# Optimization experiments

Hardware: AMD Instinct MI355X
Metric: run time of the kernel (lower is better)

## Reference

```python
import jax, jax.numpy as jnp
import numpy as np
from jax import lax

K = 512   # codebook size
D = 32    # latent dim == encoder out channels
DN = ('NCHW', 'OIHW', 'NCHW')


def _conv(x, w, b, stride):
    y = lax.conv_general_dilated(x, w, (stride, stride), ((1, 1), (1, 1)),
                                 dimension_numbers=DN)
    return y + b[None, :, None, None]


def _deconv(x, w, b):
    # torch ConvTranspose2d(k=4, s=2, p=1); weight layout (in, out, kh, kw).
    # Equivalent: conv with lhs_dilation=2, pad k-1-p = 2, spatially flipped,
    # in/out-swapped kernel.
    rhs = jnp.transpose(jnp.flip(w, (2, 3)), (1, 0, 2, 3))
    y = lax.conv_general_dilated(x, rhs, (1, 1), ((2, 2), (2, 2)),
                                 lhs_dilation=(2, 2), dimension_numbers=DN)
    return y + b[None, :, None, None]


def _forward(imgs, w1, b1, w2, b2, codebook, dw1, db1, dw2, db2):
    # Encoder
    h = jax.nn.relu(_conv(imgs, w1, b1, 2))
    z_e = jax.nn.relu(_conv(h, w2, b2, 2))          # (B, 32, H/4, W/4)
    # Vector quantize
    z = jnp.transpose(z_e, (0, 2, 3, 1))            # (B, h, w, D)
    flat = z.reshape(-1, D)                          # (N, D)
    dist = (jnp.sum(flat * flat, axis=1, keepdims=True)
            + jnp.sum(codebook * codebook, axis=1)
            - 2.0 * flat @ codebook.T)               # (N, K)
    q = jnp.argmin(dist, axis=1)                     # (N,)
    z_q = codebook[q].reshape(z.shape)               # gather == one-hot matmul
    codebook_loss = jnp.mean((lax.stop_gradient(z_q) - z) ** 2)
    commit_loss = jnp.mean((z_q - lax.stop_gradient(z)) ** 2)
    vq_loss = codebook_loss + commit_loss
    z_q_st = z + lax.stop_gradient(z_q - z)          # straight-through
    encoded = jnp.transpose(z_q_st, (0, 3, 1, 2))    # (B, 32, h, w)
    # Decoder
    d = jax.nn.relu(_deconv(encoded, dw1, db1))
    decoded = jax.nn.relu(_deconv(d, dw2, db2))
    return encoded, decoded, vq_loss


def setup_inputs() -> dict:
    key = jax.random.key(0)
    ks = jax.random.split(key, 8)

    def w_init(k, shape):
        fan_in = shape[1] * shape[2] * shape[3]
        bound = 1.0 / np.sqrt(fan_in)
        return jax.random.uniform(k, shape, jnp.float32, -bound, bound)

    imgs = jax.random.normal(ks[0], (32, 3, 256, 256), jnp.float32)
    w1 = w_init(ks[1], (16, 3, 4, 4));  b1 = jnp.zeros((16,), jnp.float32)
    w2 = w_init(ks[2], (32, 16, 4, 4)); b2 = jnp.zeros((32,), jnp.float32)
    # decoder ConvTranspose2d weights, torch layout (in, out, kh, kw)
    dw1 = w_init(ks[3], (32, 16, 4, 4)); db1 = jnp.zeros((16,), jnp.float32)
    dw2 = w_init(ks[4], (16, 3, 4, 4));  db2 = jnp.zeros((3,), jnp.float32)
    codebook = jax.random.uniform(ks[5], (K, D), jnp.float32, -1.0 / K, 1.0 / K)
    return dict(imgs=imgs, w1=w1, b1=b1, w2=w2, b2=b2, codebook=codebook,
                dw1=dw1, db1=db1, dw2=dw2, db2=db2)


def reference(imgs, w1, b1, w2, b2, codebook, dw1, db1, dw2, db2):
    return _forward(imgs, w1, b1, w2, b2, codebook, dw1, db1, dw2, db2)
```

## Files before the change

kernel.cpp:

```cpp
#include <hip/hip_runtime.h>
#include <float.h>

#pragma clang fp contract(off)

__device__ __forceinline__ float pw32(const float* p) {
  float r0 = p[0], r1 = p[1], r2 = p[2], r3 = p[3];
  float r4 = p[4], r5 = p[5], r6 = p[6], r7 = p[7];
  r0 += p[8];  r1 += p[9];  r2 += p[10]; r3 += p[11];
  r4 += p[12]; r5 += p[13]; r6 += p[14]; r7 += p[15];
  r0 += p[16]; r1 += p[17]; r2 += p[18]; r3 += p[19];
  r4 += p[20]; r5 += p[21]; r6 += p[22]; r7 += p[23];
  r0 += p[24]; r1 += p[25]; r2 += p[26]; r3 += p[27];
  r4 += p[28]; r5 += p[29]; r6 += p[30]; r7 += p[31];
  return ((r0 + r1) + (r2 + r3)) + ((r4 + r5) + (r6 + r7));
}

__global__ __launch_bounds__(256) void k_prep(
    const float* __restrict__ w1, const float* __restrict__ w2,
    const float* __restrict__ cb, float* __restrict__ w1t,
    float* __restrict__ w2t, float* __restrict__ bnG) {
  int t = threadIdx.x;
  for (int i = t; i < 8192; i += 256) {
    int tap = i >> 5, co = i & 31;
    w2t[i] = w2[co * 256 + tap];
  }
  for (int i = t; i < 768; i += 256) {
    int tap = i >> 4, co = i & 15;
    w1t[i] = w1[co * 48 + tap];
  }
  for (int k = t; k < 512; k += 256) {
    float p[32];
    #pragma unroll
    for (int d = 0; d < 32; d++) { float c = cb[k * 32 + d]; p[d] = c * c; }
    bnG[k] = pw32(p);
  }
}

__global__ __launch_bounds__(256) void k_conv1(
    const float* __restrict__ img, const float* __restrict__ w1t,
    const float* __restrict__ b1, float* __restrict__ h1, int b0) {
  int idx = blockIdx.x * 256 + threadIdx.x;
  int x  = idx & 127;
  int y  = (idx >> 7) & 127;
  int bl = idx >> 14;
  const float* im = img + (long)(b0 + bl) * 196608;
  float acc[16];
  #pragma unroll
  for (int q = 0; q < 16; q++) acc[q] = 0.f;
  int iy0 = 2 * y - 1, ix0 = 2 * x - 1;
  for (int ci = 0; ci < 3; ci++) {
    const float* imc = im + ci * 65536;
    for (int r = 0; r < 4; r++) {
      int iy = iy0 + r;
      if ((unsigned)iy >= 256u) continue;
      const float* row = imc + iy * 256;
      for (int c = 0; c < 4; c++) {
        int ix = ix0 + c;
        float hv = ((unsigned)ix < 256u) ? row[ix] : 0.f;
        const float* wp = w1t + ((ci * 16 + r * 4 + c) << 4);
        #pragma unroll
        for (int co = 0; co < 16; co++)
          acc[co] = fmaf(hv, wp[co], acc[co]);
      }
    }
  }
  long hbase = (long)bl * 262144 + y * 128 + x;
  #pragma unroll
  for (int co = 0; co < 16; co++)
    h1[hbase + (long)co * 16384] = fmaxf(acc[co] + b1[co], 0.f);
}

__global__ __launch_bounds__(256, 3) void k_conv2z(
    const float* __restrict__ h1, const float* __restrict__ w2t,
    const float* __restrict__ b2, float* __restrict__ enct, int b0) {
  int t = threadIdx.x;
  int half = blockIdx.x & 1;
  int coff = half << 4;
  int ppix = (blockIdx.x >> 1) * 256 + t;
  int x  = ppix & 63;
  int y  = (ppix >> 6) & 63;
  int bl = ppix >> 12;
  int bg = b0 + bl;

  float z[16];
  #pragma unroll
  for (int q = 0; q < 16; q++) z[q] = 0.f;

  int iy0 = 2 * y - 1, ix0 = 2 * x - 1;
  for (int ci = 0; ci < 16; ci++) {
    long hbase = (long)bl * 262144 + (long)ci * 16384;
    for (int r = 0; r < 4; r++) {
      int iy = iy0 + r;
      if ((unsigned)iy >= 128u) continue;
      const float* hrow = h1 + hbase + (long)iy * 128;
      const float* wrow = w2t + ((ci * 16 + r * 4) << 5) + coff;
      for (int c = 0; c < 4; c++) {
        int ix = ix0 + c;
        float hv = ((unsigned)ix < 128u) ? hrow[ix] : 0.f;
        const float* wp = wrow + (c << 5);
        #pragma unroll
        for (int co = 0; co < 16; co++)
          z[co] = fmaf(hv, wp[co], z[co]);
      }
    }
  }
  float4* et4 = (float4*)(enct + ((long)bg * 4096 + y * 64 + x) * 32 + coff);
  #pragma unroll
  for (int d4 = 0; d4 < 4; d4++) {
    float4 v;
    v.x = fmaxf(z[d4 * 4 + 0] + b2[coff + d4 * 4 + 0], 0.f);
    v.y = fmaxf(z[d4 * 4 + 1] + b2[coff + d4 * 4 + 1], 0.f);
    v.z = fmaxf(z[d4 * 4 + 2] + b2[coff + d4 * 4 + 2], 0.f);
    v.w = fmaxf(z[d4 * 4 + 3] + b2[coff + d4 * 4 + 3], 0.f);
    et4[d4] = v;
  }
}

template <int W>
__device__ __forceinline__ double vq_epi(const float* cw, const float (&z)[32],
                                         float* __restrict__ enc, long ebase,
                                         float4* et4) {
  int d = W * 4;
  float f0 = cw[d + 0] - z[d + 0], e0 = z[d + 0] + f0;
  float f1 = cw[d + 1] - z[d + 1], e1 = z[d + 1] + f1;
  float f2 = cw[d + 2] - z[d + 2], e2 = z[d + 2] + f2;
  float f3 = cw[d + 3] - z[d + 3], e3 = z[d + 3] + f3;
  enc[ebase + (long)(d + 0) * 4096] = e0;
  enc[ebase + (long)(d + 1) * 4096] = e1;
  enc[ebase + (long)(d + 2) * 4096] = e2;
  enc[ebase + (long)(d + 3) * 4096] = e3;
  double ls = 0.0;
  ls += (double)f0 * (double)f0;
  ls += (double)f1 * (double)f1;
  ls += (double)f2 * (double)f2;
  ls += (double)f3 * (double)f3;
  float4 v; v.x = e0; v.y = e1; v.z = e2; v.w = e3;
  et4[W] = v;
  return ls;
}

__global__ __launch_bounds__(512) void k_vq(
    const float* __restrict__ cb, const float* __restrict__ bnG,
    float* __restrict__ enc, float* enct,
    double* __restrict__ partial, int b0) {
  __shared__ float sb[512];
  __shared__ int   sq[512];
  __shared__ double sls[8];
  int t = threadIdx.x, l = t & 63;
  int w = __builtin_amdgcn_readfirstlane(t >> 6);
  int yy = blockIdx.x & 63;
  int bl = blockIdx.x >> 6;
  int bg = b0 + bl;
  long pg = (long)bg * 4096 + yy * 64 + l;

  float z[32];
  const float4* z4 = (const float4*)(enct + pg * 32);
  #pragma unroll
  for (int i = 0; i < 8; i++) {
    float4 v = z4[i];
    z[i * 4 + 0] = v.x; z[i * 4 + 1] = v.y;
    z[i * 4 + 2] = v.z; z[i * 4 + 3] = v.w;
  }
  float pz[32];
  #pragma unroll
  for (int d = 0; d < 32; d++) pz[d] = z[d] * z[d];
  float a = pw32(pz);

  int kbase = w << 6;
  float best = FLT_MAX; int bq = kbase;
  for (int k = kbase; k < kbase + 64; k += 4) {
    const float* c0 = cb + (k << 5);
    float m0 = 0.f, m1 = 0.f, m2 = 0.f, m3 = 0.f;
    #pragma unroll
    for (int d = 0; d < 32; d++) {
      m0 = fmaf(z[d], c0[d],      m0);
      m1 = fmaf(z[d], c0[32 + d], m1);
      m2 = fmaf(z[d], c0[64 + d], m2);
      m3 = fmaf(z[d], c0[96 + d], m3);
    }
    float d0 = (a + bnG[k])     - 2.0f * m0;
    float d1 = (a + bnG[k + 1]) - 2.0f * m1;
    float d2 = (a + bnG[k + 2]) - 2.0f * m2;
    float d3 = (a + bnG[k + 3]) - 2.0f * m3;
    if (d0 < best) { best = d0; bq = k; }
    if (d1 < best) { best = d1; bq = k + 1; }
    if (d2 < best) { best = d2; bq = k + 2; }
    if (d3 < best) { best = d3; bq = k + 3; }
  }
  sb[t] = best; sq[t] = bq;
  __syncthreads();
  float gb = sb[l]; int gq = sq[l];
  #pragma unroll
  for (int ww = 1; ww < 8; ww++) {
    float ob = sb[(ww << 6) + l];
    int   oq = sq[(ww << 6) + l];
    if (ob < gb) { gb = ob; gq = oq; }
  }

  const float* cw = cb + (gq << 5);
  long ebase = (long)bg * 131072 + yy * 64 + l;
  float4* et4 = (float4*)(enct + pg * 32);
  double ls;
  if      (w == 0) ls = vq_epi<0>(cw, z, enc, ebase, et4);
  else if (w == 1) ls = vq_epi<1>(cw, z, enc, ebase, et4);
  else if (w == 2) ls = vq_epi<2>(cw, z, enc, ebase, et4);
  else if (w == 3) ls = vq_epi<3>(cw, z, enc, ebase, et4);
  else if (w == 4) ls = vq_epi<4>(cw, z, enc, ebase, et4);
  else if (w == 5) ls = vq_epi<5>(cw, z, enc, ebase, et4);
  else if (w == 6) ls = vq_epi<6>(cw, z, enc, ebase, et4);
  else             ls = vq_epi<7>(cw, z, enc, ebase, et4);

  #pragma unroll
  for (int off = 32; off > 0; off >>= 1)
    ls += __shfl_down(ls, off, 64);
  if (l == 0) sls[w] = ls;
  __syncthreads();
  if (t == 0) {
    double s = sls[0];
    #pragma unroll
    for (int ww = 1; ww < 8; ww++) s += sls[ww];
    partial[(long)b0 * 64 + blockIdx.x] = s;
  }
}

__global__ __launch_bounds__(256) void k_deconv1(
    const float* __restrict__ enct, const float* __restrict__ dw1,
    const float* __restrict__ db1, float* __restrict__ d1t, int b0) {
  __shared__ float w[8192];
  for (int i = threadIdx.x; i < 8192; i += 256) {
    int co = i & 15, ci = (i >> 4) & 31, kk = i >> 9;
    w[i] = dw1[ci * 256 + co * 16 + kk];
  }
  __syncthreads();
  int idx = blockIdx.x * 256 + threadIdx.x;
  int ox = idx & 127;
  int oy = (idx >> 7) & 127;
  int bl = idx >> 14;
  int bg = b0 + bl;
  float acc[16];
  #pragma unroll
  for (int q = 0; q < 16; q++) acc[q] = 0.f;
  int iyt = (oy + 1) >> 1, ixt = (ox + 1) >> 1;
  for (int sy = 0; sy < 2; sy++) {
    int iy = iyt - sy;
    int ky = oy + 1 - 2 * iy;
    if ((unsigned)iy >= 64u || (unsigned)ky >= 4u) continue;
    for (int sx = 0; sx < 2; sx++) {
      int ix = ixt - sx;
      int kx = ox + 1 - 2 * ix;
      if ((unsigned)ix >= 64u || (unsigned)kx >= 4u) continue;
      const float4* ep4 =
          (const float4*)(enct + ((long)bg * 4096 + iy * 64 + ix) * 32);
      const float4* wl4 = (const float4*)(w + ((ky * 4 + kx) << 9));
      #pragma unroll
      for (int c4 = 0; c4 < 8; c4++) {
        float4 e = ep4[c4];
        #pragma unroll
        for (int j = 0; j < 4; j++) {
          float ev = (j == 0) ? e.x : (j == 1) ? e.y : (j == 2) ? e.z : e.w;
          int ci = c4 * 4 + j;
          #pragma unroll
          for (int q = 0; q < 4; q++) {
            float4 wv = wl4[ci * 4 + q];
            acc[q * 4 + 0] = fmaf(ev, wv.x, acc[q * 4 + 0]);
            acc[q * 4 + 1] = fmaf(ev, wv.y, acc[q * 4 + 1]);
            acc[q * 4 + 2] = fmaf(ev, wv.z, acc[q * 4 + 2]);
            acc[q * 4 + 3] = fmaf(ev, wv.w, acc[q * 4 + 3]);
          }
        }
      }
    }
  }
  float4* o4 = (float4*)(d1t + (long)idx * 16);
  #pragma unroll
  for (int q = 0; q < 4; q++) {
    float4 v;
    v.x = fmaxf(acc[q * 4 + 0] + db1[q * 4 + 0], 0.f);
    v.y = fmaxf(acc[q * 4 + 1] + db1[q * 4 + 1], 0.f);
    v.z = fmaxf(acc[q * 4 + 2] + db1[q * 4 + 2], 0.f);
    v.w = fmaxf(acc[q * 4 + 3] + db1[q * 4 + 3], 0.f);
    o4[q] = v;
  }
}

__global__ __launch_bounds__(256) void k_deconv2(
    const float* __restrict__ d1t, const float* __restrict__ dw2,
    const float* __restrict__ db2, float* __restrict__ dec, int b0) {
  __shared__ float w[768];
  for (int i = threadIdx.x; i < 768; i += 256) {
    int ci = i & 15, kk = (i >> 4) & 15, co = i >> 8;
    w[i] = dw2[ci * 48 + co * 16 + kk];
  }
  __syncthreads();
  int idx = blockIdx.x * 256 + threadIdx.x;
  int ox = idx & 255;
  int oy = (idx >> 8) & 255;
  int bl = idx >> 16;
  int bg = b0 + bl;
  float acc[3] = {0.f, 0.f, 0.f};
  int iyt = (oy + 1) >> 1, ixt = (ox + 1) >> 1;
  for (int sy = 0; sy < 2; sy++) {
    int iy = iyt - sy;
    int ky = oy + 1 - 2 * iy;
    if ((unsigned)iy >= 128u || (unsigned)ky >= 4u) continue;
    for (int sx = 0; sx < 2; sx++) {
      int ix = ixt - sx;
      int kx = ox + 1 - 2 * ix;
      if ((unsigned)ix >= 128u || (unsigned)kx >= 4u) continue;
      const float4* dp4 =
          (const float4*)(d1t + ((long)bl * 16384 + iy * 128 + ix) * 16);
      float4 dv0 = dp4[0], dv1 = dp4[1], dv2 = dp4[2], dv3 = dp4[3];
      int kk4 = (ky * 4 + kx) << 4;
      #pragma unroll
      for (int co = 0; co < 3; co++) {
        const float4* wp4 = (const float4*)(w + (co << 8) + kk4);
        float4 w0 = wp4[0], w1 = wp4[1], w2 = wp4[2], w3 = wp4[3];
        float a = acc[co];
        a = fmaf(dv0.x, w0.x, a); a = fmaf(dv0.y, w0.y, a);
        a = fmaf(dv0.z, w0.z, a); a = fmaf(dv0.w, w0.w, a);
        a = fmaf(dv1.x, w1.x, a); a = fmaf(dv1.y, w1.y, a);
        a = fmaf(dv1.z, w1.z, a); a = fmaf(dv1.w, w1.w, a);
        a = fmaf(dv2.x, w2.x, a); a = fmaf(dv2.y, w2.y, a);
        a = fmaf(dv2.z, w2.z, a); a = fmaf(dv2.w, w2.w, a);
        a = fmaf(dv3.x, w3.x, a); a = fmaf(dv3.y, w3.y, a);
        a = fmaf(dv3.z, w3.z, a); a = fmaf(dv3.w, w3.w, a);
        acc[co] = a;
      }
    }
  }
  long obase = (long)bg * 196608 + oy * 256 + ox;
  #pragma unroll
  for (int co = 0; co < 3; co++)
    dec[obase + (long)co * 65536] = fmaxf(acc[co] + db2[co], 0.f);
}

__global__ __launch_bounds__(256) void k_loss(
    const double* __restrict__ partial, float* __restrict__ out) {
  __shared__ double r[256];
  int t = threadIdx.x;
  double s = 0.0;
  for (int i = t; i < 2048; i += 256) s += partial[i];
  r[t] = s;
  __syncthreads();
  for (int st = 128; st > 0; st >>= 1) {
    if (t < st) r[t] += r[t + st];
    __syncthreads();
  }
  if (t == 0) out[0] = (float)(2.0 * r[0] / 4194304.0);
}

extern "C" void kernel_launch(void* const* d_in, const int* in_sizes, int n_in,
                              void* d_out, int out_size, void* d_ws, size_t ws_size,
                              hipStream_t stream) {
  const float* imgs = (const float*)d_in[0];
  const float* w1   = (const float*)d_in[1];
  const float* b1   = (const float*)d_in[2];
  const float* w2   = (const float*)d_in[3];
  const float* b2   = (const float*)d_in[4];
  const float* cb   = (const float*)d_in[5];
  const float* dw1  = (const float*)d_in[6];
  const float* db1  = (const float*)d_in[7];
  const float* dw2  = (const float*)d_in[8];
  const float* db2  = (const float*)d_in[9];

  float* out = (float*)d_out;
  float* enc = out;
  float* dec = out + 4194304;
  float* vql = out + 10485760;
  float* enct = dec + 2097152;

  long ws = (long)ws_size;
  long top = (ws - 16384) & ~255L;
  double* partial = (double*)((char*)d_ws + top);
  top = (top - 2048) & ~255L;
  float* bnG = (float*)((char*)d_ws + top);
  top = (top - 32768) & ~255L;
  float* w2t = (float*)((char*)d_ws + top);
  top = (top - 3072) & ~255L;
  float* w1t = (float*)((char*)d_ws + top);

  k_prep<<<1, 256, 0, stream>>>(w1, w2, cb, w1t, w2t, bnG);

  int cc = 1;
  for (int c = 32; c >= 1; c >>= 1)
    if ((long)c * 1048576 <= top) { cc = c; break; }

  float* h1 = (float*)d_ws;
  for (int b0 = 0; b0 < 32; b0 += cc) {
    k_conv1<<<cc * 64, 256, 0, stream>>>(imgs, w1t, b1, h1, b0);
    k_conv2z<<<cc * 32, 256, 0, stream>>>(h1, w2t, b2, enct, b0);
    k_vq<<<cc * 64, 512, 0, stream>>>(cb, bnG, enc, enct, partial, b0);
  }

  float* d1t = (float*)d_ws;
  for (int b0 = 0; b0 < 32; b0 += cc) {
    k_deconv1<<<cc * 64, 256, 0, stream>>>(enct, dw1, db1, d1t, b0);
    k_deconv2<<<cc * 256, 256, 0, stream>>>(d1t, dw2, db2, dec, b0);
  }

  k_loss<<<1, 256, 0, stream>>>(partial, vql);
}
```

Before: 356.0 us.

## Compute two output columns per thread in deconv1 with pre-transposed global weights

The first transposed convolution now has each thread produce an even/odd pair of output pixels in a row. The pair shares input columns, so each input vector loaded from memory serves both outputs, and the grid is halved. The per-block shared-memory weight staging and its barrier are dropped. The weights are transposed once in the prep kernel and read from global memory, relying on the cache and uniform loads. Each thread now holds twice as many accumulators and input registers, which raises register pressure and may lower occupancy.

```diff
diff --git a/kernel.cpp b/kernel.cpp
--- a/kernel.cpp
+++ b/kernel.cpp
@@ -17,8 +17,9 @@
 
 __global__ __launch_bounds__(256) void k_prep(
     const float* __restrict__ w1, const float* __restrict__ w2,
-    const float* __restrict__ cb, float* __restrict__ w1t,
-    float* __restrict__ w2t, float* __restrict__ bnG) {
+    const float* __restrict__ cb, const float* __restrict__ dw1,
+    float* __restrict__ w1t, float* __restrict__ w2t,
+    float* __restrict__ wd1t, float* __restrict__ bnG) {
   int t = threadIdx.x;
   for (int i = t; i < 8192; i += 256) {
     int tap = i >> 5, co = i & 31;
@@ -27,6 +28,10 @@
   for (int i = t; i < 768; i += 256) {
     int tap = i >> 4, co = i & 15;
     w1t[i] = w1[co * 48 + tap];
+  }
+  for (int i = t; i < 8192; i += 256) {
+    int kk = i >> 9, ci = (i >> 4) & 31, co = i & 15;
+    wd1t[i] = dw1[ci * 256 + co * 16 + kk];
   }
   for (int k = t; k < 512; k += 256) {
     float p[32];
@@ -224,62 +229,79 @@
 }
 
 __global__ __launch_bounds__(256) void k_deconv1(
-    const float* __restrict__ enct, const float* __restrict__ dw1,
+    const float* __restrict__ enct, const float* __restrict__ wd1t,
     const float* __restrict__ db1, float* __restrict__ d1t, int b0) {
-  __shared__ float w[8192];
-  for (int i = threadIdx.x; i < 8192; i += 256) {
-    int co = i & 15, ci = (i >> 4) & 31, kk = i >> 9;
-    w[i] = dw1[ci * 256 + co * 16 + kk];
-  }
-  __syncthreads();
   int idx = blockIdx.x * 256 + threadIdx.x;
-  int ox = idx & 127;
-  int oy = (idx >> 7) & 127;
-  int bl = idx >> 14;
+  int p  = idx & 63;
+  int oy = (idx >> 6) & 127;
+  int bl = idx >> 13;
   int bg = b0 + bl;
-  float acc[16];
-  #pragma unroll
-  for (int q = 0; q < 16; q++) acc[q] = 0.f;
-  int iyt = (oy + 1) >> 1, ixt = (ox + 1) >> 1;
+  float accE[16], accO[16];
+  #pragma unroll
+  for (int q = 0; q < 16; q++) { accE[q] = 0.f; accO[q] = 0.f; }
+  int iyt = (oy + 1) >> 1;
   for (int sy = 0; sy < 2; sy++) {
     int iy = iyt - sy;
+    if ((unsigned)iy >= 64u) continue;
     int ky = oy + 1 - 2 * iy;
-    if ((unsigned)iy >= 64u || (unsigned)ky >= 4u) continue;
+    long rbase = ((long)bg * 4096 + iy * 64) * 32;
     for (int sx = 0; sx < 2; sx++) {
-      int ix = ixt - sx;
-      int kx = ox + 1 - 2 * ix;
-      if ((unsigned)ix >= 64u || (unsigned)kx >= 4u) continue;
-      const float4* ep4 =
-          (const float4*)(enct + ((long)bg * 4096 + iy * 64 + ix) * 32);
-      const float4* wl4 = (const float4*)(w + ((ky * 4 + kx) << 9));
+      int colA = p - sx;
+      int colB = p + 1 - sx;
+      const float* wE = wd1t + ((ky * 4 + 1 + 2 * sx) << 9);
+      const float* wO = wd1t + ((ky * 4 + 2 * sx) << 9);
+      float4 eA[8], eB[8];
+      if ((unsigned)colA < 64u) {
+        const float4* qa = (const float4*)(enct + rbase + (long)colA * 32);
+        #pragma unroll
+        for (int i = 0; i < 8; i++) eA[i] = qa[i];
+      } else {
+        #pragma unroll
+        for (int i = 0; i < 8; i++) eA[i] = make_float4(0.f, 0.f, 0.f, 0.f);
+      }
+      if ((unsigned)colB < 64u) {
+        const float4* qb = (const float4*)(enct + rbase + (long)colB * 32);
+        #pragma unroll
+        for (int i = 0; i < 8; i++) eB[i] = qb[i];
+      } else {
+        #pragma unroll
+        for (int i = 0; i < 8; i++) eB[i] = make_float4(0.f, 0.f, 0.f, 0.f);
+      }
       #pragma unroll
       for (int c4 = 0; c4 < 8; c4++) {
-        float4 e = ep4[c4];
+        float4 a4 = eA[c4], b4 = eB[c4];
         #pragma unroll
         for (int j = 0; j < 4; j++) {
-          float ev = (j == 0) ? e.x : (j == 1) ? e.y : (j == 2) ? e.z : e.w;
+          float ea = (j == 0) ? a4.x : (j == 1) ? a4.y : (j == 2) ? a4.z : a4.w;
+          float eb = (j == 0) ? b4.x : (j == 1) ? b4.y : (j == 2) ? b4.z : b4.w;
           int ci = c4 * 4 + j;
+          const float* we = wE + (ci << 4);
+          const float* wo = wO + (ci << 4);
           #pragma unroll
-          for (int q = 0; q < 4; q++) {
-            float4 wv = wl4[ci * 4 + q];
-            acc[q * 4 + 0] = fmaf(ev, wv.x, acc[q * 4 + 0]);
-            acc[q * 4 + 1] = fmaf(ev, wv.y, acc[q * 4 + 1]);
-            acc[q * 4 + 2] = fmaf(ev, wv.z, acc[q * 4 + 2]);
-            acc[q * 4 + 3] = fmaf(ev, wv.w, acc[q * 4 + 3]);
+          for (int co = 0; co < 16; co++) {
+            accE[co] = fmaf(ea, we[co], accE[co]);
+            accO[co] = fmaf(eb, wo[co], accO[co]);
           }
         }
       }
     }
   }
-  float4* o4 = (float4*)(d1t + (long)idx * 16);
+  long pg = (long)bl * 16384 + oy * 128 + 2 * p;
+  float4* oE = (float4*)(d1t + pg * 16);
+  float4* oO = (float4*)(d1t + (pg + 1) * 16);
   #pragma unroll
   for (int q = 0; q < 4; q++) {
-    float4 v;
-    v.x = fmaxf(acc[q * 4 + 0] + db1[q * 4 + 0], 0.f);
-    v.y = fmaxf(acc[q * 4 + 1] + db1[q * 4 + 1], 0.f);
-    v.z = fmaxf(acc[q * 4 + 2] + db1[q * 4 + 2], 0.f);
-    v.w = fmaxf(acc[q * 4 + 3] + db1[q * 4 + 3], 0.f);
-    o4[q] = v;
+    float4 vE, vO;
+    vE.x = fmaxf(accE[q * 4 + 0] + db1[q * 4 + 0], 0.f);
+    vE.y = fmaxf(accE[q * 4 + 1] + db1[q * 4 + 1], 0.f);
+    vE.z = fmaxf(accE[q * 4 + 2] + db1[q * 4 + 2], 0.f);
+    vE.w = fmaxf(accE[q * 4 + 3] + db1[q * 4 + 3], 0.f);
+    vO.x = fmaxf(accO[q * 4 + 0] + db1[q * 4 + 0], 0.f);
+    vO.y = fmaxf(accO[q * 4 + 1] + db1[q * 4 + 1], 0.f);
+    vO.z = fmaxf(accO[q * 4 + 2] + db1[q * 4 + 2], 0.f);
+    vO.w = fmaxf(accO[q * 4 + 3] + db1[q * 4 + 3], 0.f);
+    oE[q] = vE;
+    oO[q] = vO;
   }
 }
 
@@ -378,8 +400,10 @@
   float* w2t = (float*)((char*)d_ws + top);
   top = (top - 3072) & ~255L;
   float* w1t = (float*)((char*)d_ws + top);
-
-  k_prep<<<1, 256, 0, stream>>>(w1, w2, cb, w1t, w2t, bnG);
+  top = (top - 32768) & ~255L;
+  float* wd1t = (float*)((char*)d_ws + top);
+
+  k_prep<<<1, 256, 0, stream>>>(w1, w2, cb, dw1, w1t, w2t, wd1t, bnG);
 
   int cc = 1;
   for (int c = 32; c >= 1; c >>= 1)
@@ -394,7 +418,7 @@
 
   float* d1t = (float*)d_ws;
   for (int b0 = 0; b0 < 32; b0 += cc) {
-    k_deconv1<<<cc * 64, 256, 0, stream>>>(enct, dw1, db1, d1t, b0);
+    k_deconv1<<<cc * 32, 256, 0, stream>>>(enct, wd1t, db1, d1t, b0);
     k_deconv2<<<cc * 256, 256, 0, stream>>>(d1t, dw2, db2, dec, b0);
   }
 
```

Result: slower. 444.8 us (+24.9%).
